# Kernel optimization log

Measured on AMD Instinct MI355X. Metric: run time of the kernel, lower is better.

The kernel has to match this reference:

```python
import jax, jax.numpy as jnp
import numpy as np

N_EMBED = 40
HEAD_SIZE = 10
N_HEADS = 4
LN_EPS = 1e-5


def _layernorm(x, g, b):
    mu = jnp.mean(x, axis=-1, keepdims=True)
    var = jnp.mean(jnp.square(x - mu), axis=-1, keepdims=True)
    return (x - mu) * jax.lax.rsqrt(var + LN_EPS) * g + b


def setup_inputs() -> dict:
    key = jax.random.key(0)
    ks = jax.random.split(key, 12)
    B, T = 16, 2048
    s = 1.0 / np.sqrt(N_EMBED)
    return {
        "x": jax.random.normal(ks[0], (B, T, N_EMBED), dtype=jnp.float32),
        # per-head Q/K/V weights stacked: [H, n_embed, head_size]
        "Wq": jax.random.normal(ks[1], (N_HEADS, N_EMBED, HEAD_SIZE), dtype=jnp.float32) * s,
        "Wk": jax.random.normal(ks[2], (N_HEADS, N_EMBED, HEAD_SIZE), dtype=jnp.float32) * s,
        "Wv": jax.random.normal(ks[3], (N_HEADS, N_EMBED, HEAD_SIZE), dtype=jnp.float32) * s,
        "Wp": jax.random.normal(ks[4], (N_EMBED, N_EMBED), dtype=jnp.float32) * s,
        "bp": jnp.zeros((N_EMBED,), dtype=jnp.float32),
        "W1": jax.random.normal(ks[5], (N_EMBED, N_EMBED), dtype=jnp.float32) * s,
        "b1": jnp.zeros((N_EMBED,), dtype=jnp.float32),
        "W2": jax.random.normal(ks[6], (N_EMBED, N_EMBED), dtype=jnp.float32) * s,
        "b2": jnp.zeros((N_EMBED,), dtype=jnp.float32),
        "g1": jnp.ones((N_EMBED,), dtype=jnp.float32),
        "be1": jnp.zeros((N_EMBED,), dtype=jnp.float32),
        "g2": jnp.ones((N_EMBED,), dtype=jnp.float32),
        "be2": jnp.zeros((N_EMBED,), dtype=jnp.float32),
    }


def reference(x, Wq, Wk, Wv, Wp, bp, W1, b1, W2, b2, g1, be1, g2, be2):
    B, T, D = x.shape
    # --- pre-norm (note: original overwrites x, so residual uses ln1(x)) ---
    x = _layernorm(x, g1, be1)
    # --- multi-head attention (faithful to source: scores = k @ q^T, no scale, no mask) ---
    q = jnp.einsum("btd,hde->bhte", x, Wq)  # [B,H,T,hs]
    k = jnp.einsum("btd,hde->bhte", x, Wk)
    v = jnp.einsum("btd,hde->bhte", x, Wv)
    w = jnp.einsum("bhie,bhje->bhij", k, q)  # k @ q.transpose(-2,-1)
    w = jax.nn.softmax(w, axis=-1)
    out = jnp.einsum("bhij,bhje->bhie", w, v)  # [B,H,T,hs]
    out = jnp.transpose(out, (0, 2, 1, 3)).reshape(B, T, D)  # concat heads
    out = out @ Wp + bp
    x = x + out
    # --- second norm + FFN (residual uses ln2(x), as in source) ---
    x = _layernorm(x, g2, be2)
    h = jax.nn.relu(x @ W1 + b1)
    x = x + (h @ W2 + b2)
    return x
```

## Files before the change

kernel.cpp:

```cpp
#include <hip/hip_runtime.h>
#include <math.h>

namespace {

using bf16x8 = __attribute__((ext_vector_type(8))) short;
using f32x4  = __attribute__((ext_vector_type(4))) float;

constexpr int D   = 40;
constexpr int HS  = 10;
constexpr int NH  = 4;
constexpr int TT  = 2048;
constexpr int BB  = 16;
constexpr int ROWS = BB * TT;
constexpr int PE  = 16;
constexpr int VR  = 11;
constexpr float LOG2E = 1.4426950408889634f;

__device__ inline unsigned short f2b(float x) {
    unsigned int u = __float_as_uint(x);
    unsigned int r = (u + 0x7fffu + ((u >> 16) & 1u)) >> 16;
    return (unsigned short)r;
}

__device__ inline f32x4 mfma32(bf16x8 a, bf16x8 b, f32x4 c) {
    return __builtin_amdgcn_mfma_f32_16x16x32_bf16(a, b, c, 0, 0, 0);
}

__device__ inline float dot40(const float* __restrict__ xr,
                              const float* __restrict__ w) {
    float s0 = 0.f, s1 = 0.f, s2 = 0.f, s3 = 0.f;
    const float4* w4 = reinterpret_cast<const float4*>(w);
    #pragma unroll
    for (int i = 0; i < 10; ++i) {
        float4 t = w4[i];
        s0 = fmaf(xr[4*i+0], t.x, s0);
        s1 = fmaf(xr[4*i+1], t.y, s1);
        s2 = fmaf(xr[4*i+2], t.z, s2);
        s3 = fmaf(xr[4*i+3], t.w, s3);
    }
    return (s0 + s1) + (s2 + s3);
}

__global__ __launch_bounds__(256) void k_ln_qkv(
    const float* __restrict__ x,  const float* __restrict__ Wq,
    const float* __restrict__ Wk, const float* __restrict__ Wv,
    const float* __restrict__ g1, const float* __restrict__ be1,
    float* __restrict__ xn, unsigned short* __restrict__ qb,
    unsigned short* __restrict__ kb, unsigned short* __restrict__ vT)
{
    __shared__ float wt_s[3*NH*HS*D];
    __shared__ float g_s[D], b_s[D];
    const int tid = threadIdx.x;
    for (int i = tid; i < NH*D*HS; i += 256) {
        const int h = i / (D*HS), r = i % (D*HS);
        const int d = r / HS, e = r % HS;
        const int to = (h*HS + e)*D + d;
        wt_s[to]              = Wq[i];
        wt_s[NH*HS*D + to]    = Wk[i];
        wt_s[2*NH*HS*D + to]  = Wv[i];
    }
    if (tid < D) { g_s[tid] = g1[tid]; b_s[tid] = be1[tid]; }
    __syncthreads();

    const int gid = blockIdx.x * 256 + tid;
    const int eh  = gid & 1;
    const int h   = (gid >> 1) & 3;
    const int row = gid >> 3;

    float xr[D];
    const float4* xp = reinterpret_cast<const float4*>(x + (size_t)row * D);
    #pragma unroll
    for (int i = 0; i < D/4; ++i) {
        float4 t4 = xp[i];
        xr[4*i+0]=t4.x; xr[4*i+1]=t4.y; xr[4*i+2]=t4.z; xr[4*i+3]=t4.w;
    }
    float mu = 0.f;
    #pragma unroll
    for (int d = 0; d < D; ++d) mu += xr[d];
    mu *= (1.f/D);
    float var = 0.f;
    #pragma unroll
    for (int d = 0; d < D; ++d) { float dd = xr[d]-mu; var += dd*dd; }
    var *= (1.f/D);
    const float rs = rsqrtf(var + 1e-5f);
    #pragma unroll
    for (int d = 0; d < D; ++d) xr[d] = (xr[d]-mu)*rs*g_s[d] + b_s[d];

    if ((gid & 7) == 0) {
        float4* xo = reinterpret_cast<float4*>(xn + (size_t)row * D);
        #pragma unroll
        for (int i = 0; i < D/4; ++i) {
            float4 t4; t4.x=xr[4*i+0]; t4.y=xr[4*i+1]; t4.z=xr[4*i+2]; t4.w=xr[4*i+3];
            xo[i] = t4;
        }
    }

    const int b = row >> 11;
    const int t = row & (TT-1);
    const int bh = b*NH + h;
    const int e0 = eh * 5;

    float aq[5], ak[5], av[5];
    #pragma unroll
    for (int e = 0; e < 5; ++e) {
        aq[e] = dot40(xr, &wt_s[(h*HS + e0 + e)*D]);
        ak[e] = dot40(xr, &wt_s[NH*HS*D + (h*HS + e0 + e)*D]);
        av[e] = dot40(xr, &wt_s[2*NH*HS*D + (h*HS + e0 + e)*D]);
    }

    float send[5], recv[5];
    #pragma unroll
    for (int j = 0; j < 5; ++j) send[j] = eh ? aq[j] : ak[j];
    #pragma unroll
    for (int j = 0; j < 5; ++j) recv[j] = __shfl_xor(send[j], 1);

    const float scale = eh ? 1.f : LOG2E;
    float lo[5], hi[5];
    #pragma unroll
    for (int j = 0; j < 5; ++j) {
        lo[j] = eh ? recv[j] : aq[j];
        hi[j] = eh ? ak[j]   : recv[j];
    }
    union { unsigned short u[PE]; uint4 v4[2]; } U;
    #pragma unroll
    for (int e = 0; e < PE; ++e)
        U.u[e] = (e < 5) ? f2b(lo[e]*scale)
               : (e < 10) ? f2b(hi[e-5]*scale) : (unsigned short)0;
    unsigned short* dst = (eh ? kb : qb) + ((size_t)bh*TT + t)*PE;
    uint4* d4 = reinterpret_cast<uint4*>(dst);
    d4[0] = U.v4[0]; d4[1] = U.v4[1];

    #pragma unroll
    for (int e = 0; e < 5; ++e)
        vT[((size_t)bh*VR + e0 + e)*TT + t] = f2b(av[e]);
    if (eh) vT[((size_t)bh*VR + HS)*TT + t] = 0x3F80;
}

__global__ __launch_bounds__(256) void k_attn(
    const unsigned short* __restrict__ qb, const unsigned short* __restrict__ kb,
    const unsigned short* __restrict__ vT, float* __restrict__ ao)
{
    __shared__ __align__(16) unsigned short PT[4][2][16][40];
    const int w    = threadIdx.x >> 6;
    const int lane = threadIdx.x & 63;
    const int g    = lane >> 4;
    const int li   = lane & 15;
    const int bh   = blockIdx.y;
    const int i0   = blockIdx.x * 64 + w * 16;
    const size_t bT = (size_t)bh * TT;

    const bf16x8 zero8 = {0,0,0,0,0,0,0,0};
    const f32x4  zacc  = {0.f,0.f,0.f,0.f};

    bf16x8 kf = zero8;
    if (g < 2) kf = *reinterpret_cast<const bf16x8*>(kb + (bT + i0 + li)*PE + 8*g);

    f32x4 accA = zacc, accB = zacc;
    const bool qok = (g < 2), vok = (li <= HS);
    const unsigned short* vrow = vT + ((size_t)bh*VR + (li <= HS ? li : 0))*TT;
    const unsigned short* qrow = qb + (bT + li)*PE + 8*g;

    bf16x8 a0A=zero8, a1A=zero8, a0B=zero8, a1B=zero8, vfA=zero8, vfB=zero8;
    if (qok) {
        a0A = *reinterpret_cast<const bf16x8*>(qrow);
        a1A = *reinterpret_cast<const bf16x8*>(qrow + (size_t)16*PE);
        a0B = *reinterpret_cast<const bf16x8*>(qrow + (size_t)(TT/2)*PE);
        a1B = *reinterpret_cast<const bf16x8*>(qrow + (size_t)(TT/2 + 16)*PE);
    }
    if (vok) {
        vfA = *reinterpret_cast<const bf16x8*>(vrow + 8*g);
        vfB = *reinterpret_cast<const bf16x8*>(vrow + TT/2 + 8*g);
    }

    for (int it = 0; it < TT/64; ++it) {
        const int nit = (it + 1) & (TT/64 - 1);
        const int njA = nit * 32;
        const int njB = njA + TT/2;

        __builtin_amdgcn_s_setprio(1);
        f32x4 sA0 = mfma32(a0A, kf, zacc);
        f32x4 sA1 = mfma32(a1A, kf, zacc);
        f32x4 sB0 = mfma32(a0B, kf, zacc);
        f32x4 sB1 = mfma32(a1B, kf, zacc);
        __builtin_amdgcn_s_setprio(0);

        bf16x8 n0A=zero8, n1A=zero8, n0B=zero8, n1B=zero8, nvA=zero8, nvB=zero8;
        if (qok) {
            n0A = *reinterpret_cast<const bf16x8*>(qrow + (size_t)(njA     )*PE);
            n1A = *reinterpret_cast<const bf16x8*>(qrow + (size_t)(njA + 16)*PE);
            n0B = *reinterpret_cast<const bf16x8*>(qrow + (size_t)(njB     )*PE);
            n1B = *reinterpret_cast<const bf16x8*>(qrow + (size_t)(njB + 16)*PE);
        }
        if (vok) {
            nvA = *reinterpret_cast<const bf16x8*>(vrow + njA + 8*g);
            nvB = *reinterpret_cast<const bf16x8*>(vrow + njB + 8*g);
        }

        const float pA0 = __builtin_amdgcn_exp2f(sA0[0]), pA1 = __builtin_amdgcn_exp2f(sA0[1]);
        const float pA2 = __builtin_amdgcn_exp2f(sA0[2]), pA3 = __builtin_amdgcn_exp2f(sA0[3]);
        const float pA4 = __builtin_amdgcn_exp2f(sA1[0]), pA5 = __builtin_amdgcn_exp2f(sA1[1]);
        const float pA6 = __builtin_amdgcn_exp2f(sA1[2]), pA7 = __builtin_amdgcn_exp2f(sA1[3]);
        const float pB0 = __builtin_amdgcn_exp2f(sB0[0]), pB1 = __builtin_amdgcn_exp2f(sB0[1]);
        const float pB2 = __builtin_amdgcn_exp2f(sB0[2]), pB3 = __builtin_amdgcn_exp2f(sB0[3]);
        const float pB4 = __builtin_amdgcn_exp2f(sB1[0]), pB5 = __builtin_amdgcn_exp2f(sB1[1]);
        const float pB6 = __builtin_amdgcn_exp2f(sB1[2]), pB7 = __builtin_amdgcn_exp2f(sB1[3]);

        unsigned int wA0,wA1,wA2,wA3, wB0,wB1,wB2,wB3;
        asm("v_cvt_pk_bf16_f32 %0, %1, %2" : "=v"(wA0) : "v"(pA0), "v"(pA1));
        asm("v_cvt_pk_bf16_f32 %0, %1, %2" : "=v"(wA1) : "v"(pA2), "v"(pA3));
        asm("v_cvt_pk_bf16_f32 %0, %1, %2" : "=v"(wA2) : "v"(pA4), "v"(pA5));
        asm("v_cvt_pk_bf16_f32 %0, %1, %2" : "=v"(wA3) : "v"(pA6), "v"(pA7));
        asm("v_cvt_pk_bf16_f32 %0, %1, %2" : "=v"(wB0) : "v"(pB0), "v"(pB1));
        asm("v_cvt_pk_bf16_f32 %0, %1, %2" : "=v"(wB1) : "v"(pB2), "v"(pB3));
        asm("v_cvt_pk_bf16_f32 %0, %1, %2" : "=v"(wB2) : "v"(pB4), "v"(pB5));
        asm("v_cvt_pk_bf16_f32 %0, %1, %2" : "=v"(wB3) : "v"(pB6), "v"(pB7));

        *reinterpret_cast<uint2*>(&PT[w][0][li][4*g])      = make_uint2(wA0, wA1);
        *reinterpret_cast<uint2*>(&PT[w][0][li][16 + 4*g]) = make_uint2(wA2, wA3);
        *reinterpret_cast<uint2*>(&PT[w][1][li][4*g])      = make_uint2(wB0, wB1);
        *reinterpret_cast<uint2*>(&PT[w][1][li][16 + 4*g]) = make_uint2(wB2, wB3);

        bf16x8 pfA = *reinterpret_cast<const bf16x8*>(&PT[w][0][li][8*g]);
        bf16x8 pfB = *reinterpret_cast<const bf16x8*>(&PT[w][1][li][8*g]);

        __builtin_amdgcn_s_setprio(1);
        accA = mfma32(vfA, pfA, accA);
        accB = mfma32(vfB, pfB, accB);
        __builtin_amdgcn_s_setprio(0);

        a0A = n0A; a1A = n1A; a0B = n0B; a1B = n1B; vfA = nvA; vfB = nvB;
    }

    const f32x4 acc = accA + accB;
    const float l = __shfl(acc[2], 32 + li);
    const float linv = 1.f / l;
    float* orow = ao + (bT + i0 + li) * HS;
    #pragma unroll
    for (int r = 0; r < 4; ++r) {
        const int e = 4*g + r;
        if (e < HS) orow[e] = acc[r] * linv;
    }
}

__global__ __launch_bounds__(256) void k_epilogue(
    const float* __restrict__ attn, const float* __restrict__ xn,
    const float* __restrict__ Wp, const float* __restrict__ bp,
    const float* __restrict__ W1, const float* __restrict__ b1,
    const float* __restrict__ W2, const float* __restrict__ b2,
    const float* __restrict__ g2, const float* __restrict__ be2,
    float* __restrict__ out)
{
    __shared__ float wp_s[D*D], w1_s[D*D], w2_s[D*D];
    __shared__ float bp_s[D], b1_s[D], b2_s[D], g_s[D], be_s[D];
    const int tid = threadIdx.x;
    for (int i = tid; i < D*D; i += 256) { wp_s[i]=Wp[i]; w1_s[i]=W1[i]; w2_s[i]=W2[i]; }
    if (tid < D) {
        bp_s[tid]=bp[tid]; b1_s[tid]=b1[tid]; b2_s[tid]=b2[tid];
        g_s[tid]=g2[tid]; be_s[tid]=be2[tid];
    }
    __syncthreads();

    const int gid  = blockIdx.x * 256 + tid;
    const int row  = gid >> 2;
    const int q4   = gid & 3;
    const int b0   = q4 * 10;
    const int lane = tid & 63;
    const int base = lane & 60;
    const int b    = row >> 11;
    const int t    = row & (TT-1);

    float cat[D];
    #pragma unroll
    for (int h = 0; h < NH; ++h) {
        const float2* ap = reinterpret_cast<const float2*>(
            attn + ((((size_t)b*NH + h)*TT) + t)*HS);
        #pragma unroll
        for (int e = 0; e < HS/2; ++e) {
            float2 t2 = ap[e];
            cat[h*HS + 2*e] = t2.x; cat[h*HS + 2*e + 1] = t2.y;
        }
    }

    float y[10];
    {
        const float2* xp = reinterpret_cast<const float2*>(xn + (size_t)row*D + b0);
        #pragma unroll
        for (int i = 0; i < 5; ++i) {
            float2 t2 = xp[i];
            y[2*i+0] = t2.x; y[2*i+1] = t2.y;
        }
    }
    #pragma unroll
    for (int d = 0; d < 10; ++d) y[d] += bp_s[b0+d];
    for (int c = 0; c < D; ++c) {
        const float cc = cat[c];
        const float* wr = &wp_s[c*D + b0];
        #pragma unroll
        for (int d = 0; d < 10; ++d) y[d] = fmaf(cc, wr[d], y[d]);
    }

    float sp = 0.f;
    #pragma unroll
    for (int d = 0; d < 10; ++d) sp += y[d];
    sp += __shfl_xor(sp, 1); sp += __shfl_xor(sp, 2);
    const float mu = sp * (1.f/D);
    float vp = 0.f;
    #pragma unroll
    for (int d = 0; d < 10; ++d) { float dd = y[d]-mu; vp += dd*dd; }
    vp += __shfl_xor(vp, 1); vp += __shfl_xor(vp, 2);
    const float rs = rsqrtf(vp * (1.f/D) + 1e-5f);

    float y2[10];
    #pragma unroll
    for (int d = 0; d < 10; ++d) y2[d] = (y[d]-mu)*rs*g_s[b0+d] + be_s[b0+d];

    float z[D];
    #pragma unroll
    for (int seg = 0; seg < 4; ++seg)
        #pragma unroll
        for (int j = 0; j < 10; ++j)
            z[seg*10 + j] = __shfl(y2[j], base + seg);

    float hd[10];
    #pragma unroll
    for (int d = 0; d < 10; ++d) hd[d] = b1_s[b0+d];
    for (int c = 0; c < D; ++c) {
        const float cc = z[c];
        const float* wr = &w1_s[c*D + b0];
        #pragma unroll
        for (int d = 0; d < 10; ++d) hd[d] = fmaf(cc, wr[d], hd[d]);
    }
    #pragma unroll
    for (int d = 0; d < 10; ++d) hd[d] = fmaxf(hd[d], 0.f);

    float hf[D];
    #pragma unroll
    for (int seg = 0; seg < 4; ++seg)
        #pragma unroll
        for (int j = 0; j < 10; ++j)
            hf[seg*10 + j] = __shfl(hd[j], base + seg);

    float ov[10];
    #pragma unroll
    for (int d = 0; d < 10; ++d) ov[d] = y2[d] + b2_s[b0+d];
    for (int c = 0; c < D; ++c) {
        const float cc = hf[c];
        const float* wr = &w2_s[c*D + b0];
        #pragma unroll
        for (int d = 0; d < 10; ++d) ov[d] = fmaf(cc, wr[d], ov[d]);
    }

    float2* op = reinterpret_cast<float2*>(out + (size_t)row*D + b0);
    #pragma unroll
    for (int i = 0; i < 5; ++i) {
        float2 t2; t2.x = ov[2*i]; t2.y = ov[2*i+1];
        op[i] = t2;
    }
}

}

extern "C" void kernel_launch(void* const* d_in, const int* in_sizes, int n_in,
                              void* d_out, int out_size, void* d_ws, size_t ws_size,
                              hipStream_t stream) {
    const float* x   = (const float*)d_in[0];
    const float* Wq  = (const float*)d_in[1];
    const float* Wk  = (const float*)d_in[2];
    const float* Wv  = (const float*)d_in[3];
    const float* Wp  = (const float*)d_in[4];
    const float* bp  = (const float*)d_in[5];
    const float* W1  = (const float*)d_in[6];
    const float* b1  = (const float*)d_in[7];
    const float* W2  = (const float*)d_in[8];
    const float* b2  = (const float*)d_in[9];
    const float* g1  = (const float*)d_in[10];
    const float* be1 = (const float*)d_in[11];
    const float* g2  = (const float*)d_in[12];
    const float* be2 = (const float*)d_in[13];

    const size_t N = (size_t)ROWS * D;
    float* xn = (float*)d_ws;
    float* ao = xn + N;
    unsigned short* qb = (unsigned short*)(ao + N);
    unsigned short* kb = qb + (size_t)BB*NH*TT*PE;
    unsigned short* vT = kb + (size_t)BB*NH*TT*PE;

    k_ln_qkv<<<ROWS*8/256, 256, 0, stream>>>(x, Wq, Wk, Wv, g1, be1, xn, qb, kb, vT);
    k_attn<<<dim3(TT/64, BB*NH), 256, 0, stream>>>(qb, kb, vT, ao);
    k_epilogue<<<ROWS*4/256, 256, 0, stream>>>(ao, xn, Wp, bp, W1, b1, W2, b2, g2, be2,
                                               (float*)d_out);
}
```

Baseline: 117.2 us.

## Replace LDS transpose of attention probabilities with cross-lane shuffles

```diff
diff --git a/kernel.cpp b/kernel.cpp
--- a/kernel.cpp
+++ b/kernel.cpp
@@ -13,6 +13,7 @@
 constexpr int BB  = 16;
 constexpr int ROWS = BB * TT;
 constexpr int PE  = 16;
+constexpr int PE2 = 32;
 constexpr int VR  = 11;
 constexpr float LOG2E = 1.4426950408889634f;
 
@@ -126,9 +127,14 @@
     for (int e = 0; e < PE; ++e)
         U.u[e] = (e < 5) ? f2b(lo[e]*scale)
                : (e < 10) ? f2b(hi[e-5]*scale) : (unsigned short)0;
-    unsigned short* dst = (eh ? kb : qb) + ((size_t)bh*TT + t)*PE;
-    uint4* d4 = reinterpret_cast<uint4*>(dst);
-    d4[0] = U.v4[0]; d4[1] = U.v4[1];
+    if (eh) {
+        uint4* d4 = reinterpret_cast<uint4*>(kb + ((size_t)bh*TT + t)*PE);
+        d4[0] = U.v4[0]; d4[1] = U.v4[1];
+    } else {
+        uint4* d4 = reinterpret_cast<uint4*>(qb + ((size_t)bh*TT + t)*PE2);
+        d4[0] = U.v4[0]; d4[1] = U.v4[1];
+        d4[2] = make_uint4(0,0,0,0); d4[3] = make_uint4(0,0,0,0);
+    }
 
     #pragma unroll
     for (int e = 0; e < 5; ++e)
@@ -140,7 +146,6 @@
     const unsigned short* __restrict__ qb, const unsigned short* __restrict__ kb,
     const unsigned short* __restrict__ vT, float* __restrict__ ao)
 {
-    __shared__ __align__(16) unsigned short PT[4][2][16][40];
     const int w    = threadIdx.x >> 6;
     const int lane = threadIdx.x & 63;
     const int g    = lane >> 4;
@@ -155,83 +160,75 @@
     bf16x8 kf = zero8;
     if (g < 2) kf = *reinterpret_cast<const bf16x8*>(kb + (bT + i0 + li)*PE + 8*g);
 
-    f32x4 accA = zacc, accB = zacc;
-    const bool qok = (g < 2), vok = (li <= HS);
-    const unsigned short* vrow = vT + ((size_t)bh*VR + (li <= HS ? li : 0))*TT;
-    const unsigned short* qrow = qb + (bT + li)*PE + 8*g;
-
-    bf16x8 a0A=zero8, a1A=zero8, a0B=zero8, a1B=zero8, vfA=zero8, vfB=zero8;
-    if (qok) {
-        a0A = *reinterpret_cast<const bf16x8*>(qrow);
-        a1A = *reinterpret_cast<const bf16x8*>(qrow + (size_t)16*PE);
-        a0B = *reinterpret_cast<const bf16x8*>(qrow + (size_t)(TT/2)*PE);
-        a1B = *reinterpret_cast<const bf16x8*>(qrow + (size_t)(TT/2 + 16)*PE);
-    }
-    if (vok) {
-        vfA = *reinterpret_cast<const bf16x8*>(vrow + 8*g);
-        vfB = *reinterpret_cast<const bf16x8*>(vrow + TT/2 + 8*g);
-    }
-
-    for (int it = 0; it < TT/64; ++it) {
-        const int nit = (it + 1) & (TT/64 - 1);
-        const int njA = nit * 32;
-        const int njB = njA + TT/2;
-
-        __builtin_amdgcn_s_setprio(1);
-        f32x4 sA0 = mfma32(a0A, kf, zacc);
-        f32x4 sA1 = mfma32(a1A, kf, zacc);
-        f32x4 sB0 = mfma32(a0B, kf, zacc);
-        f32x4 sB1 = mfma32(a1B, kf, zacc);
-        __builtin_amdgcn_s_setprio(0);
-
-        bf16x8 n0A=zero8, n1A=zero8, n0B=zero8, n1B=zero8, nvA=zero8, nvB=zero8;
-        if (qok) {
-            n0A = *reinterpret_cast<const bf16x8*>(qrow + (size_t)(njA     )*PE);
-            n1A = *reinterpret_cast<const bf16x8*>(qrow + (size_t)(njA + 16)*PE);
-            n0B = *reinterpret_cast<const bf16x8*>(qrow + (size_t)(njB     )*PE);
-            n1B = *reinterpret_cast<const bf16x8*>(qrow + (size_t)(njB + 16)*PE);
-        }
-        if (vok) {
-            nvA = *reinterpret_cast<const bf16x8*>(vrow + njA + 8*g);
-            nvB = *reinterpret_cast<const bf16x8*>(vrow + njB + 8*g);
-        }
-
-        const float pA0 = __builtin_amdgcn_exp2f(sA0[0]), pA1 = __builtin_amdgcn_exp2f(sA0[1]);
-        const float pA2 = __builtin_amdgcn_exp2f(sA0[2]), pA3 = __builtin_amdgcn_exp2f(sA0[3]);
-        const float pA4 = __builtin_amdgcn_exp2f(sA1[0]), pA5 = __builtin_amdgcn_exp2f(sA1[1]);
-        const float pA6 = __builtin_amdgcn_exp2f(sA1[2]), pA7 = __builtin_amdgcn_exp2f(sA1[3]);
-        const float pB0 = __builtin_amdgcn_exp2f(sB0[0]), pB1 = __builtin_amdgcn_exp2f(sB0[1]);
-        const float pB2 = __builtin_amdgcn_exp2f(sB0[2]), pB3 = __builtin_amdgcn_exp2f(sB0[3]);
-        const float pB4 = __builtin_amdgcn_exp2f(sB1[0]), pB5 = __builtin_amdgcn_exp2f(sB1[1]);
-        const float pB6 = __builtin_amdgcn_exp2f(sB1[2]), pB7 = __builtin_amdgcn_exp2f(sB1[3]);
-
-        unsigned int wA0,wA1,wA2,wA3, wB0,wB1,wB2,wB3;
-        asm("v_cvt_pk_bf16_f32 %0, %1, %2" : "=v"(wA0) : "v"(pA0), "v"(pA1));
-        asm("v_cvt_pk_bf16_f32 %0, %1, %2" : "=v"(wA1) : "v"(pA2), "v"(pA3));
-        asm("v_cvt_pk_bf16_f32 %0, %1, %2" : "=v"(wA2) : "v"(pA4), "v"(pA5));
-        asm("v_cvt_pk_bf16_f32 %0, %1, %2" : "=v"(wA3) : "v"(pA6), "v"(pA7));
-        asm("v_cvt_pk_bf16_f32 %0, %1, %2" : "=v"(wB0) : "v"(pB0), "v"(pB1));
-        asm("v_cvt_pk_bf16_f32 %0, %1, %2" : "=v"(wB1) : "v"(pB2), "v"(pB3));
-        asm("v_cvt_pk_bf16_f32 %0, %1, %2" : "=v"(wB2) : "v"(pB4), "v"(pB5));
-        asm("v_cvt_pk_bf16_f32 %0, %1, %2" : "=v"(wB3) : "v"(pB6), "v"(pB7));
-
-        *reinterpret_cast<uint2*>(&PT[w][0][li][4*g])      = make_uint2(wA0, wA1);
-        *reinterpret_cast<uint2*>(&PT[w][0][li][16 + 4*g]) = make_uint2(wA2, wA3);
-        *reinterpret_cast<uint2*>(&PT[w][1][li][4*g])      = make_uint2(wB0, wB1);
-        *reinterpret_cast<uint2*>(&PT[w][1][li][16 + 4*g]) = make_uint2(wB2, wB3);
-
-        bf16x8 pfA = *reinterpret_cast<const bf16x8*>(&PT[w][0][li][8*g]);
-        bf16x8 pfB = *reinterpret_cast<const bf16x8*>(&PT[w][1][li][8*g]);
-
-        __builtin_amdgcn_s_setprio(1);
-        accA = mfma32(vfA, pfA, accA);
-        accB = mfma32(vfB, pfB, accB);
-        __builtin_amdgcn_s_setprio(0);
-
-        a0A = n0A; a1A = n1A; a0B = n0B; a1B = n1B; vfA = nvA; vfB = nvB;
-    }
-
-    const f32x4 acc = accA + accB;
+    f32x4 acc0 = zacc, acc1 = zacc;
+    const int vr = (li < VR) ? li : (VR - 1);
+    const unsigned short* vrow = vT + ((size_t)bh*VR + vr)*TT + 8*g;
+    const unsigned short* qrow = qb + (bT + li)*PE2 + 8*g;
+    const bool glo  = (g < 2);
+    const int  srcA = ((2*g) & 3) * 16 + li;
+    const int  srcB = srcA + 16;
+
+    #pragma unroll 1
+    for (int jt = 0; jt < TT; jt += 64) {
+        {
+            bf16x8 a0 = *reinterpret_cast<const bf16x8*>(qrow + (size_t)(jt     )*PE2);
+            bf16x8 a1 = *reinterpret_cast<const bf16x8*>(qrow + (size_t)(jt + 16)*PE2);
+            bf16x8 vf = *reinterpret_cast<const bf16x8*>(vrow + jt);
+            f32x4 s0 = mfma32(a0, kf, zacc);
+            f32x4 s1 = mfma32(a1, kf, zacc);
+
+            const float p0 = __builtin_amdgcn_exp2f(s0[0]), p1 = __builtin_amdgcn_exp2f(s0[1]);
+            const float p2 = __builtin_amdgcn_exp2f(s0[2]), p3 = __builtin_amdgcn_exp2f(s0[3]);
+            const float p4 = __builtin_amdgcn_exp2f(s1[0]), p5 = __builtin_amdgcn_exp2f(s1[1]);
+            const float p6 = __builtin_amdgcn_exp2f(s1[2]), p7 = __builtin_amdgcn_exp2f(s1[3]);
+            unsigned int t0w0, t0w1, t1w0, t1w1;
+            asm("v_cvt_pk_bf16_f32 %0, %1, %2" : "=v"(t0w0) : "v"(p0), "v"(p1));
+            asm("v_cvt_pk_bf16_f32 %0, %1, %2" : "=v"(t0w1) : "v"(p2), "v"(p3));
+            asm("v_cvt_pk_bf16_f32 %0, %1, %2" : "=v"(t1w0) : "v"(p4), "v"(p5));
+            asm("v_cvt_pk_bf16_f32 %0, %1, %2" : "=v"(t1w1) : "v"(p6), "v"(p7));
+
+            const unsigned int x0A = __shfl(t0w0, srcA), x1A = __shfl(t0w1, srcA);
+            const unsigned int x0B = __shfl(t0w0, srcB), x1B = __shfl(t0w1, srcB);
+            const unsigned int y0A = __shfl(t1w0, srcA), y1A = __shfl(t1w1, srcA);
+            const unsigned int y0B = __shfl(t1w0, srcB), y1B = __shfl(t1w1, srcB);
+            union { uint4 u; bf16x8 v; } B;
+            B.u.x = glo ? x0A : y0A;
+            B.u.y = glo ? x1A : y1A;
+            B.u.z = glo ? x0B : y0B;
+            B.u.w = glo ? x1B : y1B;
+            acc0 = mfma32(vf, B.v, acc0);
+        }
+        {
+            bf16x8 a0 = *reinterpret_cast<const bf16x8*>(qrow + (size_t)(jt + 32)*PE2);
+            bf16x8 a1 = *reinterpret_cast<const bf16x8*>(qrow + (size_t)(jt + 48)*PE2);
+            bf16x8 vf = *reinterpret_cast<const bf16x8*>(vrow + jt + 32);
+            f32x4 s0 = mfma32(a0, kf, zacc);
+            f32x4 s1 = mfma32(a1, kf, zacc);
+
+            const float p0 = __builtin_amdgcn_exp2f(s0[0]), p1 = __builtin_amdgcn_exp2f(s0[1]);
+            const float p2 = __builtin_amdgcn_exp2f(s0[2]), p3 = __builtin_amdgcn_exp2f(s0[3]);
+            const float p4 = __builtin_amdgcn_exp2f(s1[0]), p5 = __builtin_amdgcn_exp2f(s1[1]);
+            const float p6 = __builtin_amdgcn_exp2f(s1[2]), p7 = __builtin_amdgcn_exp2f(s1[3]);
+            unsigned int t0w0, t0w1, t1w0, t1w1;
+            asm("v_cvt_pk_bf16_f32 %0, %1, %2" : "=v"(t0w0) : "v"(p0), "v"(p1));
+            asm("v_cvt_pk_bf16_f32 %0, %1, %2" : "=v"(t0w1) : "v"(p2), "v"(p3));
+            asm("v_cvt_pk_bf16_f32 %0, %1, %2" : "=v"(t1w0) : "v"(p4), "v"(p5));
+            asm("v_cvt_pk_bf16_f32 %0, %1, %2" : "=v"(t1w1) : "v"(p6), "v"(p7));
+
+            const unsigned int x0A = __shfl(t0w0, srcA), x1A = __shfl(t0w1, srcA);
+            const unsigned int x0B = __shfl(t0w0, srcB), x1B = __shfl(t0w1, srcB);
+            const unsigned int y0A = __shfl(t1w0, srcA), y1A = __shfl(t1w1, srcA);
+            const unsigned int y0B = __shfl(t1w0, srcB), y1B = __shfl(t1w1, srcB);
+            union { uint4 u; bf16x8 v; } B;
+            B.u.x = glo ? x0A : y0A;
+            B.u.y = glo ? x1A : y1A;
+            B.u.z = glo ? x0B : y0B;
+            B.u.w = glo ? x1B : y1B;
+            acc1 = mfma32(vf, B.v, acc1);
+        }
+    }
+
+    const f32x4 acc = acc0 + acc1;
     const float l = __shfl(acc[2], 32 + li);
     const float linv = 1.f / l;
     float* orow = ao + (bT + i0 + li) * HS;
@@ -382,7 +379,7 @@
     float* xn = (float*)d_ws;
     float* ao = xn + N;
     unsigned short* qb = (unsigned short*)(ao + N);
-    unsigned short* kb = qb + (size_t)BB*NH*TT*PE;
+    unsigned short* kb = qb + (size_t)BB*NH*TT*PE2;
     unsigned short* vT = kb + (size_t)BB*NH*TT*PE;
 
     k_ln_qkv<<<ROWS*8/256, 256, 0, stream>>>(x, Wq, Wk, Wv, g1, be1, xn, qb, kb, vT);
```

New measurement: 169.8 us. 1.45x slower.

## Simplify attention loop to a single stream with unroll and occupancy hint

Applied to the files above, without the earlier changes.

```diff
diff --git a/kernel.cpp b/kernel.cpp
--- a/kernel.cpp
+++ b/kernel.cpp
@@ -136,11 +136,11 @@
     if (eh) vT[((size_t)bh*VR + HS)*TT + t] = 0x3F80;
 }
 
-__global__ __launch_bounds__(256) void k_attn(
+__global__ __launch_bounds__(256, 4) void k_attn(
     const unsigned short* __restrict__ qb, const unsigned short* __restrict__ kb,
     const unsigned short* __restrict__ vT, float* __restrict__ ao)
 {
-    __shared__ __align__(16) unsigned short PT[4][2][16][40];
+    __shared__ __align__(16) unsigned short PT[4][16][40];
     const int w    = threadIdx.x >> 6;
     const int lane = threadIdx.x & 63;
     const int g    = lane >> 4;
@@ -155,83 +155,38 @@
     bf16x8 kf = zero8;
     if (g < 2) kf = *reinterpret_cast<const bf16x8*>(kb + (bT + i0 + li)*PE + 8*g);
 
-    f32x4 accA = zacc, accB = zacc;
-    const bool qok = (g < 2), vok = (li <= HS);
+    f32x4 acc = zacc;
     const unsigned short* vrow = vT + ((size_t)bh*VR + (li <= HS ? li : 0))*TT;
-    const unsigned short* qrow = qb + (bT + li)*PE + 8*g;
-
-    bf16x8 a0A=zero8, a1A=zero8, a0B=zero8, a1B=zero8, vfA=zero8, vfB=zero8;
-    if (qok) {
-        a0A = *reinterpret_cast<const bf16x8*>(qrow);
-        a1A = *reinterpret_cast<const bf16x8*>(qrow + (size_t)16*PE);
-        a0B = *reinterpret_cast<const bf16x8*>(qrow + (size_t)(TT/2)*PE);
-        a1B = *reinterpret_cast<const bf16x8*>(qrow + (size_t)(TT/2 + 16)*PE);
-    }
-    if (vok) {
-        vfA = *reinterpret_cast<const bf16x8*>(vrow + 8*g);
-        vfB = *reinterpret_cast<const bf16x8*>(vrow + TT/2 + 8*g);
-    }
-
-    for (int it = 0; it < TT/64; ++it) {
-        const int nit = (it + 1) & (TT/64 - 1);
-        const int njA = nit * 32;
-        const int njB = njA + TT/2;
-
-        __builtin_amdgcn_s_setprio(1);
-        f32x4 sA0 = mfma32(a0A, kf, zacc);
-        f32x4 sA1 = mfma32(a1A, kf, zacc);
-        f32x4 sB0 = mfma32(a0B, kf, zacc);
-        f32x4 sB1 = mfma32(a1B, kf, zacc);
-        __builtin_amdgcn_s_setprio(0);
-
-        bf16x8 n0A=zero8, n1A=zero8, n0B=zero8, n1B=zero8, nvA=zero8, nvB=zero8;
-        if (qok) {
-            n0A = *reinterpret_cast<const bf16x8*>(qrow + (size_t)(njA     )*PE);
-            n1A = *reinterpret_cast<const bf16x8*>(qrow + (size_t)(njA + 16)*PE);
-            n0B = *reinterpret_cast<const bf16x8*>(qrow + (size_t)(njB     )*PE);
-            n1B = *reinterpret_cast<const bf16x8*>(qrow + (size_t)(njB + 16)*PE);
+
+    #pragma unroll 2
+    for (int jt = 0; jt < TT; jt += 32) {
+        bf16x8 a0 = zero8, a1 = zero8;
+        if (g < 2) {
+            a0 = *reinterpret_cast<const bf16x8*>(qb + (bT + jt      + li)*PE + 8*g);
+            a1 = *reinterpret_cast<const bf16x8*>(qb + (bT + jt + 16 + li)*PE + 8*g);
         }
-        if (vok) {
-            nvA = *reinterpret_cast<const bf16x8*>(vrow + njA + 8*g);
-            nvB = *reinterpret_cast<const bf16x8*>(vrow + njB + 8*g);
-        }
-
-        const float pA0 = __builtin_amdgcn_exp2f(sA0[0]), pA1 = __builtin_amdgcn_exp2f(sA0[1]);
-        const float pA2 = __builtin_amdgcn_exp2f(sA0[2]), pA3 = __builtin_amdgcn_exp2f(sA0[3]);
-        const float pA4 = __builtin_amdgcn_exp2f(sA1[0]), pA5 = __builtin_amdgcn_exp2f(sA1[1]);
-        const float pA6 = __builtin_amdgcn_exp2f(sA1[2]), pA7 = __builtin_amdgcn_exp2f(sA1[3]);
-        const float pB0 = __builtin_amdgcn_exp2f(sB0[0]), pB1 = __builtin_amdgcn_exp2f(sB0[1]);
-        const float pB2 = __builtin_amdgcn_exp2f(sB0[2]), pB3 = __builtin_amdgcn_exp2f(sB0[3]);
-        const float pB4 = __builtin_amdgcn_exp2f(sB1[0]), pB5 = __builtin_amdgcn_exp2f(sB1[1]);
-        const float pB6 = __builtin_amdgcn_exp2f(sB1[2]), pB7 = __builtin_amdgcn_exp2f(sB1[3]);
-
-        unsigned int wA0,wA1,wA2,wA3, wB0,wB1,wB2,wB3;
-        asm("v_cvt_pk_bf16_f32 %0, %1, %2" : "=v"(wA0) : "v"(pA0), "v"(pA1));
-        asm("v_cvt_pk_bf16_f32 %0, %1, %2" : "=v"(wA1) : "v"(pA2), "v"(pA3));
-        asm("v_cvt_pk_bf16_f32 %0, %1, %2" : "=v"(wA2) : "v"(pA4), "v"(pA5));
-        asm("v_cvt_pk_bf16_f32 %0, %1, %2" : "=v"(wA3) : "v"(pA6), "v"(pA7));
-        asm("v_cvt_pk_bf16_f32 %0, %1, %2" : "=v"(wB0) : "v"(pB0), "v"(pB1));
-        asm("v_cvt_pk_bf16_f32 %0, %1, %2" : "=v"(wB1) : "v"(pB2), "v"(pB3));
-        asm("v_cvt_pk_bf16_f32 %0, %1, %2" : "=v"(wB2) : "v"(pB4), "v"(pB5));
-        asm("v_cvt_pk_bf16_f32 %0, %1, %2" : "=v"(wB3) : "v"(pB6), "v"(pB7));
-
-        *reinterpret_cast<uint2*>(&PT[w][0][li][4*g])      = make_uint2(wA0, wA1);
-        *reinterpret_cast<uint2*>(&PT[w][0][li][16 + 4*g]) = make_uint2(wA2, wA3);
-        *reinterpret_cast<uint2*>(&PT[w][1][li][4*g])      = make_uint2(wB0, wB1);
-        *reinterpret_cast<uint2*>(&PT[w][1][li][16 + 4*g]) = make_uint2(wB2, wB3);
-
-        bf16x8 pfA = *reinterpret_cast<const bf16x8*>(&PT[w][0][li][8*g]);
-        bf16x8 pfB = *reinterpret_cast<const bf16x8*>(&PT[w][1][li][8*g]);
-
-        __builtin_amdgcn_s_setprio(1);
-        accA = mfma32(vfA, pfA, accA);
-        accB = mfma32(vfB, pfB, accB);
-        __builtin_amdgcn_s_setprio(0);
-
-        a0A = n0A; a1A = n1A; a0B = n0B; a1B = n1B; vfA = nvA; vfB = nvB;
-    }
-
-    const f32x4 acc = accA + accB;
+        f32x4 s0 = __builtin_amdgcn_mfma_f32_16x16x32_bf16(a0, kf, zacc, 0, 0, 0);
+        f32x4 s1 = __builtin_amdgcn_mfma_f32_16x16x32_bf16(a1, kf, zacc, 0, 0, 0);
+
+        const float p0 = __builtin_amdgcn_exp2f(s0[0]), p1 = __builtin_amdgcn_exp2f(s0[1]);
+        const float p2 = __builtin_amdgcn_exp2f(s0[2]), p3 = __builtin_amdgcn_exp2f(s0[3]);
+        const float p4 = __builtin_amdgcn_exp2f(s1[0]), p5 = __builtin_amdgcn_exp2f(s1[1]);
+        const float p6 = __builtin_amdgcn_exp2f(s1[2]), p7 = __builtin_amdgcn_exp2f(s1[3]);
+
+        unsigned int w0, w1, w2, w3;
+        asm("v_cvt_pk_bf16_f32 %0, %1, %2" : "=v"(w0) : "v"(p0), "v"(p1));
+        asm("v_cvt_pk_bf16_f32 %0, %1, %2" : "=v"(w1) : "v"(p2), "v"(p3));
+        asm("v_cvt_pk_bf16_f32 %0, %1, %2" : "=v"(w2) : "v"(p4), "v"(p5));
+        asm("v_cvt_pk_bf16_f32 %0, %1, %2" : "=v"(w3) : "v"(p6), "v"(p7));
+        *reinterpret_cast<uint2*>(&PT[w][li][4*g])      = make_uint2(w0, w1);
+        *reinterpret_cast<uint2*>(&PT[w][li][16 + 4*g]) = make_uint2(w2, w3);
+
+        bf16x8 pf = *reinterpret_cast<const bf16x8*>(&PT[w][li][8*g]);
+        bf16x8 vf = zero8;
+        if (li <= HS) vf = *reinterpret_cast<const bf16x8*>(vrow + jt + 8*g);
+        acc = __builtin_amdgcn_mfma_f32_16x16x32_bf16(vf, pf, acc, 0, 0, 0);
+    }
+
     const float l = __shfl(acc[2], 32 + li);
     const float linv = 1.f / l;
     float* orow = ao + (bT + i0 + li) * HS;
```

Result: faster. 113.5 us (-3.1%).
